# Optimization experiments

Hardware: AMD Instinct MI355X
Metric: run time of the kernel (lower is better)

Reference implementation:

```python
import jax, jax.numpy as jnp
import numpy as np

L = 7
D = 20
V = 2 ** L                      # voxel_size
NUM_EMB = V ** 3
DOM_LO, DOM_HI = -1.0, 1.0
DOM_LEN = DOM_HI - DOM_LO

# 8 corner offsets in the order used by the torch module
OFFSETS = jnp.array([[0, 0, 0], [1, 0, 0], [0, 1, 0], [1, 1, 0],
                     [0, 0, 1], [1, 0, 1], [0, 1, 1], [1, 1, 1]], dtype=jnp.int32)


def setup_inputs() -> dict:
    key = jax.random.key(0)
    kx, kg = jax.random.split(key)
    # points strictly inside the domain so floor()+1 corner stays in-range
    x = jax.random.uniform(kx, (1_000_000, 3), jnp.float32, minval=-1.0, maxval=0.998)
    grid = jax.random.normal(kg, (NUM_EMB, D), jnp.float32) * 0.02  # embedding table
    return {"x": x, "grid": grid}


def reference(x, grid):
    # points -> grid space, floor to lower corner
    gp = jnp.floor((x - DOM_LO) / DOM_LEN * V)                  # [P,3] float
    grid_idx = gp[:, None, :].astype(jnp.int32) + OFFSETS[None]  # [P,8,3]
    # flat index: ix * V^0 + iy * V^1 + iz * V^2
    flat = grid_idx[..., 0] + grid_idx[..., 1] * V + grid_idx[..., 2] * (V * V)
    Q_emb = grid[flat]                                          # [P,8,D] gather
    Q_pos = grid_idx.astype(x.dtype) / V * DOM_LEN + DOM_LO      # [P,8,3] world pos

    px, py, pz = x[:, 0], x[:, 1], x[:, 2]
    x1, x2 = Q_pos[:, 0, 0], Q_pos[:, 1, 0]
    y1, y2 = Q_pos[:, 0, 1], Q_pos[:, 2, 1]
    z1, z2 = Q_pos[:, 0, 2], Q_pos[:, 4, 2]

    q000, q100, q010, q110 = Q_emb[:, 0], Q_emb[:, 1], Q_emb[:, 2], Q_emb[:, 3]
    q001, q101, q011, q111 = Q_emb[:, 4], Q_emb[:, 5], Q_emb[:, 6], Q_emb[:, 7]

    wx0 = ((x2 - px) / (x2 - x1))[:, None]
    wx1 = ((px - x1) / (x2 - x1))[:, None]
    fx0 = wx0 * q000 + wx1 * q100
    fx1 = wx0 * q010 + wx1 * q110
    fx2 = wx0 * q001 + wx1 * q101
    fx3 = wx0 * q011 + wx1 * q111

    wy0 = ((y2 - py) / (y2 - y1))[:, None]
    wy1 = ((py - y1) / (y2 - y1))[:, None]
    fy0 = wy0 * fx0 + wy1 * fx1
    fy1 = wy0 * fx2 + wy1 * fx3

    wz0 = ((z2 - pz) / (z2 - z1))[:, None]
    wz1 = ((pz - z1) / (z2 - z1))[:, None]
    return wz0 * fy0 + wz1 * fy1                                 # [P,D]
```

## Files before the change

### kernel.cpp

```cpp
#include <hip/hip_runtime.h>

#define V 128
#define D 20
#define NUM_EMB (V * V * V)

typedef float v4f __attribute__((ext_vector_type(4)));

__global__ __launch_bounds__(320) void dense_grid_enc_kernel(
    const float* __restrict__ x, const float* __restrict__ grid,
    float* __restrict__ out, int N)
{
    int tid = threadIdx.x;
    int lp  = tid / 5;
    int k   = tid - lp * 5;
    int i   = blockIdx.x * 64 + lp;
    if (i >= N) return;

    float px = x[3 * i + 0];
    float py = x[3 * i + 1];
    float pz = x[3 * i + 2];

    int ix = (int)floorf((px + 1.0f) * 64.0f);
    int iy = (int)floorf((py + 1.0f) * 64.0f);
    int iz = (int)floorf((pz + 1.0f) * 64.0f);

    float x1 = (float)ix * (2.0f / 128.0f) - 1.0f;
    float x2 = (float)(ix + 1) * (2.0f / 128.0f) - 1.0f;
    float y1 = (float)iy * (2.0f / 128.0f) - 1.0f;
    float y2 = (float)(iy + 1) * (2.0f / 128.0f) - 1.0f;
    float z1 = (float)iz * (2.0f / 128.0f) - 1.0f;
    float z2 = (float)(iz + 1) * (2.0f / 128.0f) - 1.0f;

    float wx1 = (px - x1) * 64.0f, wx0 = (x2 - px) * 64.0f;
    float wy1 = (py - y1) * 64.0f, wy0 = (y2 - py) * 64.0f;
    float wz1 = (pz - z1) * 64.0f, wz0 = (z2 - pz) * 64.0f;

    int f000 = ix + iy * V + iz * V * V;

    int flats[8];
    flats[0] = f000;
    flats[1] = f000 + 1;
    flats[2] = f000 + V;
    flats[3] = f000 + V + 1;
    flats[4] = f000 + V * V;
    flats[5] = f000 + V * V + 1;
    flats[6] = f000 + V * V + V;
    flats[7] = f000 + V * V + V + 1;

    #pragma unroll
    for (int c = 0; c < 8; c++) {
        if (flats[c] > NUM_EMB - 1) flats[c] = NUM_EMB - 1;
    }

    float w[8];
    w[0] = wx0 * wy0 * wz0;
    w[1] = wx1 * wy0 * wz0;
    w[2] = wx0 * wy1 * wz0;
    w[3] = wx1 * wy1 * wz0;
    w[4] = wx0 * wy0 * wz1;
    w[5] = wx1 * wy0 * wz1;
    w[6] = wx0 * wy1 * wz1;
    w[7] = wx1 * wy1 * wz1;

    v4f q[8];
    #pragma unroll
    for (int c = 0; c < 8; c++) {
        q[c] = *(const v4f*)(grid + (size_t)flats[c] * D + 4 * k);
    }

    v4f acc = (v4f)(0.0f);
    #pragma unroll
    for (int c = 0; c < 8; c++) {
        acc += w[c] * q[c];
    }

    __builtin_nontemporal_store(acc, (v4f*)(out + (size_t)i * D + 4 * k));
}

extern "C" void kernel_launch(void* const* d_in, const int* in_sizes, int n_in,
                              void* d_out, int out_size, void* d_ws, size_t ws_size,
                              hipStream_t stream) {
    const float* x = (const float*)d_in[0];
    const float* grid = (const float*)d_in[1];
    float* out = (float*)d_out;
    int N = in_sizes[0] / 3;

    int pts_per_block = 64;
    int nblocks = (N + pts_per_block - 1) / pts_per_block;
    dense_grid_enc_kernel<<<nblocks, 320, 0, stream>>>(x, grid, out, N);
}
```

Baseline: 363.0 us.

## Bin points into spatial buckets before gathering to improve grid locality

Adds a binning pass that assigns each point to one of 4096 8x8x8-voxel buckets via atomics and writes point indices to a workspace. A second kernel processes one bucket per block, so gathers from the 168MB grid hit nearby rows and reuse cache lines in L2. Overflowing buckets are computed directly in the bin pass. The cost is an extra memset, atomic contention, index writes and reads, and scattered output stores and x reads.

After: 416.0 us. +14.6%, slower.

```diff
diff --git a/kernel.cpp b/kernel.cpp
--- a/kernel.cpp
+++ b/kernel.cpp
@@ -3,19 +3,16 @@
 #define V 128
 #define D 20
 #define NUM_EMB (V * V * V)
+#define NBUCK 4096
+#define BCAP  512
 
 typedef float v4f __attribute__((ext_vector_type(4)));
+typedef unsigned int u32;
 
-__global__ __launch_bounds__(320) void dense_grid_enc_kernel(
+__device__ __forceinline__ void compute_chunk(
     const float* __restrict__ x, const float* __restrict__ grid,
-    float* __restrict__ out, int N)
+    float* __restrict__ out, int i, int k)
 {
-    int tid = threadIdx.x;
-    int lp  = tid / 5;
-    int k   = tid - lp * 5;
-    int i   = blockIdx.x * 64 + lp;
-    if (i >= N) return;
-
     float px = x[3 * i + 0];
     float py = x[3 * i + 1];
     float pz = x[3 * i + 2];
@@ -77,6 +74,64 @@
     __builtin_nontemporal_store(acc, (v4f*)(out + (size_t)i * D + 4 * k));
 }
 
+__global__ __launch_bounds__(256) void bin_kernel(
+    const float* __restrict__ x, const float* __restrict__ grid,
+    float* __restrict__ out, u32* __restrict__ cnt, u32* __restrict__ bucket,
+    int N)
+{
+    int i = blockIdx.x * 256 + threadIdx.x;
+    if (i >= N) return;
+    float px = x[3 * i + 0];
+    float py = x[3 * i + 1];
+    float pz = x[3 * i + 2];
+    int ix = (int)floorf((px + 1.0f) * 64.0f);
+    int iy = (int)floorf((py + 1.0f) * 64.0f);
+    int iz = (int)floorf((pz + 1.0f) * 64.0f);
+    int b = (ix >> 3) + ((iy >> 3) << 4) + ((iz >> 3) << 8);
+    u32 pos = atomicAdd(&cnt[b], 1u);
+    if (pos < BCAP) {
+        bucket[(size_t)b * BCAP + pos] = (u32)i;
+    } else {
+        for (int k = 0; k < 5; k++) compute_chunk(x, grid, out, i, k);
+    }
+}
+
+__global__ __launch_bounds__(320) void gather_kernel(
+    const float* __restrict__ x, const float* __restrict__ grid,
+    float* __restrict__ out, const u32* __restrict__ cnt,
+    const u32* __restrict__ bucket)
+{
+    int bid = blockIdx.x;
+    int b = (bid & 7) * (NBUCK / 8) + (bid >> 3);
+
+    u32 n = cnt[b];
+    if (n > BCAP) n = BCAP;
+
+    int tid = threadIdx.x;
+    int lp  = tid / 5;
+    int k   = tid - lp * 5;
+
+    for (u32 base = 0; base < n; base += 64) {
+        u32 p = base + (u32)lp;
+        if (p < n) {
+            int i = (int)bucket[(size_t)b * BCAP + p];
+            compute_chunk(x, grid, out, i, k);
+        }
+    }
+}
+
+__global__ __launch_bounds__(320) void naive_kernel(
+    const float* __restrict__ x, const float* __restrict__ grid,
+    float* __restrict__ out, int N)
+{
+    int tid = threadIdx.x;
+    int lp  = tid / 5;
+    int k   = tid - lp * 5;
+    int i   = blockIdx.x * 64 + lp;
+    if (i >= N) return;
+    compute_chunk(x, grid, out, i, k);
+}
+
 extern "C" void kernel_launch(void* const* d_in, const int* in_sizes, int n_in,
                               void* d_out, int out_size, void* d_ws, size_t ws_size,
                               hipStream_t stream) {
@@ -85,7 +140,17 @@
     float* out = (float*)d_out;
     int N = in_sizes[0] / 3;
 
-    int pts_per_block = 64;
-    int nblocks = (N + pts_per_block - 1) / pts_per_block;
-    dense_grid_enc_kernel<<<nblocks, 320, 0, stream>>>(x, grid, out, N);
+    size_t need = (size_t)NBUCK * 4 + (size_t)NBUCK * BCAP * 4;
+    if (d_ws == nullptr || ws_size < need) {
+        int nblocks = (N + 63) / 64;
+        naive_kernel<<<nblocks, 320, 0, stream>>>(x, grid, out, N);
+        return;
+    }
+
+    u32* cnt = (u32*)d_ws;
+    u32* bucket = cnt + NBUCK;
+
+    hipMemsetAsync(cnt, 0, (size_t)NBUCK * 4, stream);
+    bin_kernel<<<(N + 255) / 256, 256, 0, stream>>>(x, grid, out, cnt, bucket, N);
+    gather_kernel<<<NBUCK, 320, 0, stream>>>(x, grid, out, cnt, bucket);
 }
```
